# Kernel tuning notes

Hardware: AMD Instinct MI355X
Metric: run time of the kernel (lower is better)

Reference implementation:

```python
import jax, jax.numpy as jnp
import numpy as np
from jax import lax

IN_CH = 128
INTER_CH = 128
AUDIO_CH = 1
K = 2
DILATIONS = [2 ** i for i in range(10)] * 4  # 40 blocks
B, T = 4, 8192


def _causal_conv1d(x, w, dilation):
    # x: [B, Cin, T], w: [Cout, Cin, K] -> [B, Cout, T], left-padded (causal)
    pad = dilation * (w.shape[-1] - 1)
    return lax.conv_general_dilated(
        x, w, window_strides=(1,), padding=[(pad, 0)],
        rhs_dilation=(dilation,), dimension_numbers=('NCH', 'OIH', 'NCH'))


def setup_inputs() -> dict:
    key = jax.random.key(0)
    ks = jax.random.split(key, 12)
    L = len(DILATIONS)
    s = 0.05
    return {
        'x': jax.random.normal(ks[0], (B, AUDIO_CH, T), jnp.float32),
        'pre_w': jax.random.normal(ks[1], (IN_CH, AUDIO_CH, 3), jnp.float32) * s,
        'pre_b': jax.random.normal(ks[2], (IN_CH,), jnp.float32) * s,
        'conv_w': jax.random.normal(ks[3], (L, 2 * INTER_CH, IN_CH, K), jnp.float32) * s,
        'conv_b': jax.random.normal(ks[4], (L, 2 * INTER_CH), jnp.float32) * s,
        'post_w': jax.random.normal(ks[5], (L, IN_CH, INTER_CH), jnp.float32) * s,
        'post_b': jax.random.normal(ks[6], (L, IN_CH), jnp.float32) * s,
        'lin1_w': jax.random.normal(ks[7], (INTER_CH, INTER_CH), jnp.float32) * s,
        'lin1_b': jax.random.normal(ks[8], (INTER_CH,), jnp.float32) * s,
        'lin2_w': jax.random.normal(ks[9], (IN_CH, INTER_CH), jnp.float32) * s,
        'lin2_b': jax.random.normal(ks[10], (IN_CH,), jnp.float32) * s,
    }


def reference(x, pre_w, pre_b, conv_w, conv_b, post_w, post_b,
              lin1_w, lin1_b, lin2_w, lin2_b):
    # pre_net: ConstantPad1d((2,0)) + Conv1d(k=3) == causal conv, dilation 1
    h = _causal_conv1d(x, pre_w, 1) + pre_b[None, :, None]  # [B, IN_CH, T]
    skip_sum = jnp.zeros((x.shape[0], INTER_CH, x.shape[-1]), h.dtype)
    for i, d in enumerate(DILATIONS):
        y = _causal_conv1d(h, conv_w[i], d) + conv_b[i][None, :, None]  # [B, 2*INTER, T]
        a, b = jnp.split(y, 2, axis=1)
        skip = a * jax.nn.sigmoid(b)                                    # GLU
        h = h + jnp.einsum('oc,bct->bot', post_w[i], skip) + post_b[i][None, :, None]
        skip_sum = skip_sum + skip
    # conv2sa: [B, C, T] -> [T, B, C]
    z = jnp.transpose(skip_sum, (2, 0, 1))
    z = jax.nn.relu(z)
    z = z @ lin1_w.T + lin1_b
    z = jax.nn.relu(z)
    return z @ lin2_w.T + lin2_b  # [T, B, IN_CH]
```

## Files before the change

kernel.cpp:

```cpp
#include <hip/hip_runtime.h>
#include <hip/hip_bf16.h>

typedef __bf16 bf16;
typedef unsigned long long u64;
typedef __bf16 bf16x8 __attribute__((ext_vector_type(8)));
typedef __bf16 bf16x4 __attribute__((ext_vector_type(4)));
typedef float f32x4 __attribute__((ext_vector_type(4)));

#define NB 4
#define T 8192
#define C 128
#define NBLK 40
#define XS 136

#define MFMA(a, b, c) __builtin_amdgcn_mfma_f32_16x16x32_bf16(a, b, c, 0, 0, 0)

__device__ __forceinline__ float bf2f(bf16 x){ return (float)x; }
__device__ __forceinline__ bf16 f2bf(float x){ return (bf16)x; }

__device__ __forceinline__ float ld(const void* p, int i, int isbf){
    return isbf ? bf2f(((const bf16*)p)[i]) : ((const float*)p)[i];
}

__device__ __forceinline__ bf16x4 ld8(const bf16* p){
    u64 v = __hip_atomic_load((const u64*)p, __ATOMIC_RELAXED, __HIP_MEMORY_SCOPE_AGENT);
    return __builtin_bit_cast(bf16x4, v);
}
__device__ __forceinline__ void st16c(bf16* p, f32x4 v){
    asm volatile("global_store_dwordx4 %0, %1, off sc0 sc1" :: "v"(p), "v"(v) : "memory");
}

__global__ __launch_bounds__(64) void k_detect(const unsigned short* __restrict__ u,
                                               int* __restrict__ flag){
    unsigned short v = u[threadIdx.x * 2];
    int e = (v >> 7) & 255;
    bool sane = (e >= 100 && e <= 140) || ((v & 0x7FFF) == 0);
    unsigned long long m = __ballot(sane);
    if (threadIdx.x == 0) *flag = (__popcll(m) >= 48) ? 1 : 0;
}

__global__ __launch_bounds__(256) void k_prep(
    const void* __restrict__ conv_w, const void* __restrict__ post_w,
    const void* __restrict__ lin1_w, const void* __restrict__ lin2_w,
    const void* __restrict__ x,      const void* __restrict__ conv_b,
    const void* __restrict__ post_b, const void* __restrict__ pre_w,
    const void* __restrict__ pre_b,  const void* __restrict__ lin1_b,
    const void* __restrict__ lin2_b,
    bf16* __restrict__ weff, bf16* __restrict__ pwc,
    bf16* __restrict__ w1c,  bf16* __restrict__ w2c,
    float* __restrict__ xc,  float* __restrict__ cbf,
    float* __restrict__ pbf, float* __restrict__ misc,
    const int* __restrict__ flag){
    int f = *flag;
    int g = blockIdx.x * 256 + threadIdx.x;
    if (g < 327680){
        int blk = g >> 13, r = g & 8191, o = r >> 5, j = r & 31;
        int k = (j >= 16) ? 1 : 0;
        int base = blk * 65536 + o * 256 + (j * 8 - k * 128) * 2 + k;
        bf16x8 v;
#pragma unroll
        for (int m = 0; m < 8; m++) v[m] = f2bf(ld(conv_w, base + m * 2, f));
        *(bf16x8*)(weff + (size_t)g * 8) = v;
    } else if (g < 409600){
        int e = (g - 327680) * 8;
        bf16x8 v;
#pragma unroll
        for (int m = 0; m < 8; m++) v[m] = f2bf(ld(post_w, e + m, f));
        *(bf16x8*)(pwc + e) = v;
    } else if (g < 411648){
        int e = (g - 409600) * 8;
        bf16x8 v;
#pragma unroll
        for (int m = 0; m < 8; m++) v[m] = f2bf(ld(lin1_w, e + m, f));
        *(bf16x8*)(w1c + e) = v;
    } else if (g < 413696){
        int e = (g - 411648) * 8;
        bf16x8 v;
#pragma unroll
        for (int m = 0; m < 8; m++) v[m] = f2bf(ld(lin2_w, e + m, f));
        *(bf16x8*)(w2c + e) = v;
    } else if (g < 417792){
        int e = (g - 413696) * 8;
#pragma unroll
        for (int m = 0; m < 8; m++) xc[e + m] = ld(x, e + m, f);
    } else if (g < 419072){
        int e = (g - 417792) * 8;
#pragma unroll
        for (int m = 0; m < 8; m++) cbf[e + m] = ld(conv_b, e + m, f);
    } else if (g < 419712){
        int e = (g - 419072) * 8;
#pragma unroll
        for (int m = 0; m < 8; m++) pbf[e + m] = ld(post_b, e + m, f);
    } else if (g < 419808){
        int e = (g - 419712) * 8;
#pragma unroll
        for (int m = 0; m < 8; m++){
            int idx = e + m;
            if      (idx < 384) misc[idx] = ld(pre_w,  idx,       f);
            else if (idx < 512) misc[idx] = ld(pre_b,  idx - 384, f);
            else if (idx < 640) misc[idx] = ld(lin1_b, idx - 512, f);
            else                misc[idx] = ld(lin2_b, idx - 640, f);
        }
    }
}

__device__ __forceinline__ void wait_ge(unsigned* p, unsigned v){
    int guard = 0;
    while (__hip_atomic_load(p, __ATOMIC_RELAXED, __HIP_MEMORY_SCOPE_AGENT) < v){
        __builtin_amdgcn_s_sleep(1);
        if (++guard > (1 << 22)) break;
    }
    asm volatile("" ::: "memory");
}

__device__ __forceinline__ void tail_store(const bf16* Xo, bf16* dst, int nrows, int tid){
    int ngr = nrows * 16;
    for (int g = tid; g < ngr; g += 512){
        int rr = 128 - nrows + (g >> 4), co = (g & 15) * 8;
        f32x4 v = *(const f32x4*)(Xo + rr * XS + co);
        st16c(dst + (size_t)rr * C + co, v);
    }
    asm volatile("s_waitcnt vmcnt(0)" ::: "memory");
}

__global__ __launch_bounds__(512, 2) void k_main(
    const float* __restrict__ xc,  const float* __restrict__ misc,
    const bf16* __restrict__ weff, const float* __restrict__ cbf,
    const bf16* __restrict__ pwc,  const float* __restrict__ pbf,
    const bf16* __restrict__ w1c,  const bf16* __restrict__ w2c,
    bf16* __restrict__ hA, bf16* __restrict__ hB,
    unsigned* __restrict__ prog, unsigned* __restrict__ cons,
    void* __restrict__ outv, const int* __restrict__ flag)
{
    __shared__ __align__(16) bf16 LDSB[3 * 128 * XS];
    bf16* Xo = LDSB;
    bf16* Xh = LDSB + 128 * XS;
    bf16* Xs = LDSB + 256 * XS;

    int tid  = threadIdx.x;
    int wg   = blockIdx.x;
    int b    = wg >> 6;
    int slab = wg & 63;
    int t0   = slab * 128;
    int wv = tid >> 6, ln = tid & 63, lo = ln & 15, quad = ln >> 4;
    const size_t hb = (size_t)b * T * C;

    float hreg[32];
    float ssum[32];

    {
        const float* xr = xc + b * T;
#pragma unroll
        for (int ct = 0; ct < 8; ct++){
            int t = t0 + ct * 16 + lo;
            float x0 = (t >= 2) ? xr[t - 2] : 0.f;
            float x1 = (t >= 1) ? xr[t - 1] : 0.f;
            float x2 = xr[t];
            bf16x4 hv;
#pragma unroll
            for (int r = 0; r < 4; r++){
                int c = wv * 16 + quad * 4 + r;
                float acc = misc[384 + c] + misc[c*3]*x0 + misc[c*3+1]*x1 + misc[c*3+2]*x2;
                hreg[ct * 4 + r] = acc;
                hv[r] = f2bf(acc);
            }
            *(bf16x4*)(Xo + (ct * 16 + lo) * XS + wv * 16 + quad * 4) = hv;
        }
    }
#pragma unroll
    for (int i = 0; i < 32; i++) ssum[i] = 0.f;
    __syncthreads();
    if (slab < 63) tail_store(Xo, hA + hb + (size_t)t0 * C, 1, tid);
    __syncthreads();
    if (tid == 0)
        __hip_atomic_store(prog + wg, 1u, __ATOMIC_RELAXED, __HIP_MEMORY_SCOPE_AGENT);

    for (int i = 0; i < NBLK; i++){
        int d  = 1 << (i % 10);
        int D  = (d >= 128) ? (d >> 7) : 1;
        int dn = (i < NBLK - 1) ? (1 << ((i + 1) % 10)) : 0;
        int Dn = (dn >= 128) ? (dn >> 7) : 1;
        int nst = (dn < 128) ? dn : 128;
        bool last = (i == NBLK - 1);
        bool do_store = !last && (slab + Dn <= 63);
        const bf16* hin  = (i & 1) ? hB : hA;
        bf16*       hout = (i & 1) ? hA : hB;
        const bf16* wb   = weff + ((size_t)i << 16);
        const bf16* pwb  = pwc  + i * 16384;
        const float* cb  = cbf + i * 256;
        const float* pb  = pbf + i * 128;

        f32x4 cacc0[8] = {}, cacc1[8] = {};

#pragma unroll
        for (int kk = 0; kk < 4; kk++){
            int ko = 128 + kk * 32 + quad * 8;
            bf16x8 a0 = *(const bf16x8*)(wb + (size_t)(wv*16 + lo) * 256 + ko);
            bf16x8 a1 = *(const bf16x8*)(wb + (size_t)(128 + wv*16 + lo) * 256 + ko);
#pragma unroll
            for (int ct = 0; ct < 8; ct++){
                bf16x8 bf_ = *(const bf16x8*)(Xo + (ct*16 + lo) * XS + kk*32 + quad*8);
                cacc0[ct] = MFMA(a0, bf_, cacc0[ct]);
                cacc1[ct] = MFMA(a1, bf_, cacc1[ct]);
            }
        }
        if (slab >= D) wait_ge(prog + (wg - D), (unsigned)(i + 1));
        {
            int nr = (d < 128) ? d : 128;
            int tbase = t0 - d;
            int ngr8 = nr * 32;
            for (int g = tid; g < ngr8; g += 512){
                int row = g >> 5, c4 = (g & 31) << 2;
                int t = tbase + row;
                bf16x4 v = {};
                if (t >= 0) v = ld8(hin + hb + (size_t)t * C + c4);
                *(bf16x4*)(Xh + row * XS + c4) = v;
            }
        }
        __syncthreads();
        if (!last && tid == 0)
            __hip_atomic_store(cons + wg, (unsigned)(i + 1),
                               __ATOMIC_RELAXED, __HIP_MEMORY_SCOPE_AGENT);
        {
            int soff[8];
#pragma unroll
            for (int ct = 0; ct < 8; ct++){
                int row = ct * 16 + lo;
                soff[ct] = (row >= d) ? (row - d) * XS
                                      : (128 * XS + row * XS);
            }
#pragma unroll
            for (int kk = 0; kk < 4; kk++){
                int ko = kk * 32 + quad * 8;
                bf16x8 a0 = *(const bf16x8*)(wb + (size_t)(wv*16 + lo) * 256 + ko);
                bf16x8 a1 = *(const bf16x8*)(wb + (size_t)(128 + wv*16 + lo) * 256 + ko);
#pragma unroll
                for (int ct = 0; ct < 8; ct++){
                    bf16x8 bf_ = *(const bf16x8*)(LDSB + soff[ct] + ko);
                    cacc0[ct] = MFMA(a0, bf_, cacc0[ct]);
                    cacc1[ct] = MFMA(a1, bf_, cacc1[ct]);
                }
            }
        }
#pragma unroll
        for (int ct = 0; ct < 8; ct++){
            int col = ct * 16 + lo;
            bf16x4 sv;
#pragma unroll
            for (int r = 0; r < 4; r++){
                int j = wv * 16 + quad * 4 + r;
                float a = cacc0[ct][r] + cb[j];
                float g = cacc1[ct][r] + cb[128 + j];
                float s = a * __builtin_amdgcn_rcpf(1.f + __expf(-g));
                ssum[ct * 4 + r] += s;
                sv[r] = f2bf(s);
            }
            if (!last) *(bf16x4*)(Xs + col * XS + wv * 16 + quad * 4) = sv;
        }
        if (last) break;
        __syncthreads();
        {
            f32x4 pacc[8] = {};
#pragma unroll
            for (int kk = 0; kk < 4; kk++){
                bf16x8 pa = *(const bf16x8*)(pwb + (wv*16 + lo) * 128 + kk*32 + quad*8);
#pragma unroll
                for (int ct = 0; ct < 8; ct++){
                    bf16x8 pbv = *(const bf16x8*)(Xs + (ct*16 + lo) * XS + kk*32 + quad*8);
                    pacc[ct] = MFMA(pa, pbv, pacc[ct]);
                }
            }
#pragma unroll
            for (int ct = 0; ct < 8; ct++){
                bf16x4 hv;
#pragma unroll
                for (int r = 0; r < 4; r++){
                    hreg[ct * 4 + r] += pacc[ct][r] + pb[wv * 16 + quad * 4 + r];
                    hv[r] = f2bf(hreg[ct * 4 + r]);
                }
                *(bf16x4*)(Xo + (ct * 16 + lo) * XS + wv * 16 + quad * 4) = hv;
            }
        }
        if (do_store && i >= 1){
            int dp = 1 << ((i - 1) % 10);
            int Dp = (dp >= 128) ? (dp >> 7) : 1;
            if (slab + Dp <= 63) wait_ge(cons + (wg + Dp), (unsigned)i);
        }
        __syncthreads();
        if (do_store) tail_store(Xo, hout + hb + (size_t)t0 * C, nst, tid);
        __syncthreads();
        if (tid == 0)
            __hip_atomic_store(prog + wg, (unsigned)(i + 2),
                               __ATOMIC_RELAXED, __HIP_MEMORY_SCOPE_AGENT);
    }

    const float* b1 = misc + 512;
    const float* b2 = misc + 640;
    int isbf = *flag;
    __syncthreads();
#pragma unroll
    for (int ct = 0; ct < 8; ct++){
        int col = ct * 16 + lo;
        bf16x4 zv;
#pragma unroll
        for (int r = 0; r < 4; r++){
            float z = ssum[ct * 4 + r];
            zv[r] = f2bf(z > 0.f ? z : 0.f);
        }
        *(bf16x4*)(Xs + col * XS + wv * 16 + quad * 4) = zv;
    }
    __syncthreads();
    f32x4 a1[8] = {};
#pragma unroll
    for (int kk = 0; kk < 4; kk++){
        bf16x8 pa = *(const bf16x8*)(w1c + (wv*16 + lo) * 128 + kk*32 + quad*8);
#pragma unroll
        for (int ct = 0; ct < 8; ct++){
            bf16x8 pbv = *(const bf16x8*)(Xs + (ct*16 + lo) * XS + kk*32 + quad*8);
            a1[ct] = MFMA(pa, pbv, a1[ct]);
        }
    }
    __syncthreads();
#pragma unroll
    for (int ct = 0; ct < 8; ct++){
        int col = ct * 16 + lo;
        bf16x4 uv;
#pragma unroll
        for (int r = 0; r < 4; r++){
            int row = wv * 16 + quad * 4 + r;
            float u = a1[ct][r] + b1[row];
            uv[r] = f2bf(u > 0.f ? u : 0.f);
        }
        *(bf16x4*)(Xs + col * XS + wv * 16 + quad * 4) = uv;
    }
    __syncthreads();
    f32x4 a2[8] = {};
#pragma unroll
    for (int kk = 0; kk < 4; kk++){
        bf16x8 pa = *(const bf16x8*)(w2c + (wv*16 + lo) * 128 + kk*32 + quad*8);
#pragma unroll
        for (int ct = 0; ct < 8; ct++){
            bf16x8 pbv = *(const bf16x8*)(Xs + (ct*16 + lo) * XS + kk*32 + quad*8);
            a2[ct] = MFMA(pa, pbv, a2[ct]);
        }
    }
#pragma unroll
    for (int ct = 0; ct < 8; ct++){
        int col = t0 + ct * 16 + lo;
#pragma unroll
        for (int r = 0; r < 4; r++){
            int row = wv * 16 + quad * 4 + r;
            float v = a2[ct][r] + b2[row];
            size_t oi = ((size_t)col * NB + b) * C + row;
            if (isbf) ((bf16*)outv)[oi] = f2bf(v);
            else      ((float*)outv)[oi] = v;
        }
    }
}

extern "C" void kernel_launch(void* const* d_in, const int* in_sizes, int n_in,
                              void* d_out, int out_size, void* d_ws, size_t ws_size,
                              hipStream_t stream){
    const void* x      = d_in[0];
    const void* pre_w  = d_in[1];
    const void* pre_b  = d_in[2];
    const void* conv_w = d_in[3];
    const void* conv_b = d_in[4];
    const void* post_w = d_in[5];
    const void* post_b = d_in[6];
    const void* lin1w  = d_in[7];
    const void* lin1b  = d_in[8];
    const void* lin2w  = d_in[9];
    const void* lin2b  = d_in[10];

    char* ws = (char*)d_ws;
    bf16*     hA   = (bf16*)    (ws);
    bf16*     hB   = (bf16*)    (ws +  8388608);
    bf16*     weff = (bf16*)    (ws + 16777216);
    bf16*     pwc  = (bf16*)    (ws + 22020096);
    bf16*     w1c  = (bf16*)    (ws + 23330816);
    bf16*     w2c  = (bf16*)    (ws + 23363584);
    float*    xc   = (float*)   (ws + 23396352);
    float*    cbf  = (float*)   (ws + 23527424);
    float*    pbf  = (float*)   (ws + 23568384);
    float*    misc = (float*)   (ws + 23588864);
    int*      flag = (int*)     (ws + 23591936);
    unsigned* prog = (unsigned*)(ws + 23592960);
    unsigned* cons = (unsigned*)(ws + 23593984);

    hipMemsetAsync(prog, 0, 2048, stream);
    k_detect<<<1, 64, 0, stream>>>((const unsigned short*)x, flag);
    k_prep<<<1640, 256, 0, stream>>>(conv_w, post_w, lin1w, lin2w, x, conv_b,
                                     post_b, pre_w, pre_b, lin1b, lin2b,
                                     weff, pwc, w1c, w2c, xc, cbf, pbf, misc, flag);

    const float* xc_c   = xc;   const float* misc_c = misc;
    const bf16*  weff_c = weff; const float* cbf_c  = cbf;
    const bf16*  pwc_c  = pwc;  const float* pbf_c  = pbf;
    const bf16*  w1c_c  = w1c;  const bf16*  w2c_c  = w2c;
    void* out_v = d_out;        const int* flag_c = flag;
    void* ka[14] = { &xc_c, &misc_c, &weff_c, &cbf_c, &pwc_c, &pbf_c,
                     &w1c_c, &w2c_c, &hA, &hB, &prog, &cons, &out_v, &flag_c };
    hipLaunchCooperativeKernel((void*)k_main, dim3(256), dim3(512), ka, 0, stream);
}
```

Measured before the change: 540.2 us.

## Prefetch halo rows and conv weights before MFMA; fold dtype detect into prep

Moves the dependency wait and the global halo-row loads ahead of the current-tap MFMA loop, keeping them in registers so their latency overlaps compute before they are written to LDS. Also preloads the shifted-tap conv weights into registers once rather than reloading them inside the second MFMA loop. Separately, folds the dtype-detection kernel into k_prep, so each block computes the flag itself and one launch is dropped. The register staging raises VGPR pressure in a 512-thread cooperative kernel, which could spill. Waiting earlier may also stall before independent compute.

```diff
diff --git a/kernel.cpp b/kernel.cpp
--- a/kernel.cpp
+++ b/kernel.cpp
@@ -28,15 +28,6 @@
 }
 __device__ __forceinline__ void st16c(bf16* p, f32x4 v){
     asm volatile("global_store_dwordx4 %0, %1, off sc0 sc1" :: "v"(p), "v"(v) : "memory");
-}
-
-__global__ __launch_bounds__(64) void k_detect(const unsigned short* __restrict__ u,
-                                               int* __restrict__ flag){
-    unsigned short v = u[threadIdx.x * 2];
-    int e = (v >> 7) & 255;
-    bool sane = (e >= 100 && e <= 140) || ((v & 0x7FFF) == 0);
-    unsigned long long m = __ballot(sane);
-    if (threadIdx.x == 0) *flag = (__popcll(m) >= 48) ? 1 : 0;
 }
 
 __global__ __launch_bounds__(256) void k_prep(
@@ -50,8 +41,21 @@
     bf16* __restrict__ w1c,  bf16* __restrict__ w2c,
     float* __restrict__ xc,  float* __restrict__ cbf,
     float* __restrict__ pbf, float* __restrict__ misc,
-    const int* __restrict__ flag){
-    int f = *flag;
+    int* __restrict__ flag){
+    __shared__ int sf;
+    if (threadIdx.x < 64){
+        unsigned short v = ((const unsigned short*)x)[threadIdx.x * 2];
+        int e = (v >> 7) & 255;
+        bool sane = (e >= 100 && e <= 140) || ((v & 0x7FFF) == 0);
+        unsigned long long m = __ballot(sane);
+        if (threadIdx.x == 0){
+            int fv = (__popcll(m) >= 48) ? 1 : 0;
+            sf = fv;
+            if (blockIdx.x == 0) *flag = fv;
+        }
+    }
+    __syncthreads();
+    int f = sf;
     int g = blockIdx.x * 256 + threadIdx.x;
     if (g < 327680){
         int blk = g >> 13, r = g & 8191, o = r >> 5, j = r & 31;
@@ -192,6 +196,30 @@
 
         f32x4 cacc0[8] = {}, cacc1[8] = {};
 
+        if (slab >= D) wait_ge(prog + (wg - D), (unsigned)(i + 1));
+        int nr = (d < 128) ? d : 128;
+        int ngr8 = nr * 32;
+        int tbase = t0 - d;
+        bf16x4 stg[8];
+#pragma unroll
+        for (int j = 0; j < 8; j++){
+            int g = j * 512 + tid;
+            bf16x4 v = {};
+            if (g < ngr8){
+                int row = g >> 5, c4 = (g & 31) << 2;
+                int t = tbase + row;
+                if (t >= 0) v = ld8(hin + hb + (size_t)t * C + c4);
+            }
+            stg[j] = v;
+        }
+        bf16x8 cw0[4], cw1[4];
+#pragma unroll
+        for (int kk = 0; kk < 4; kk++){
+            int ko = kk * 32 + quad * 8;
+            cw0[kk] = *(const bf16x8*)(wb + (size_t)(wv*16 + lo) * 256 + ko);
+            cw1[kk] = *(const bf16x8*)(wb + (size_t)(128 + wv*16 + lo) * 256 + ko);
+        }
+
 #pragma unroll
         for (int kk = 0; kk < 4; kk++){
             int ko = 128 + kk * 32 + quad * 8;
@@ -204,17 +232,12 @@
                 cacc1[ct] = MFMA(a1, bf_, cacc1[ct]);
             }
         }
-        if (slab >= D) wait_ge(prog + (wg - D), (unsigned)(i + 1));
-        {
-            int nr = (d < 128) ? d : 128;
-            int tbase = t0 - d;
-            int ngr8 = nr * 32;
-            for (int g = tid; g < ngr8; g += 512){
+#pragma unroll
+        for (int j = 0; j < 8; j++){
+            int g = j * 512 + tid;
+            if (g < ngr8){
                 int row = g >> 5, c4 = (g & 31) << 2;
-                int t = tbase + row;
-                bf16x4 v = {};
-                if (t >= 0) v = ld8(hin + hb + (size_t)t * C + c4);
-                *(bf16x4*)(Xh + row * XS + c4) = v;
+                *(bf16x4*)(Xh + row * XS + c4) = stg[j];
             }
         }
         __syncthreads();
@@ -232,13 +255,11 @@
 #pragma unroll
             for (int kk = 0; kk < 4; kk++){
                 int ko = kk * 32 + quad * 8;
-                bf16x8 a0 = *(const bf16x8*)(wb + (size_t)(wv*16 + lo) * 256 + ko);
-                bf16x8 a1 = *(const bf16x8*)(wb + (size_t)(128 + wv*16 + lo) * 256 + ko);
 #pragma unroll
                 for (int ct = 0; ct < 8; ct++){
                     bf16x8 bf_ = *(const bf16x8*)(LDSB + soff[ct] + ko);
-                    cacc0[ct] = MFMA(a0, bf_, cacc0[ct]);
-                    cacc1[ct] = MFMA(a1, bf_, cacc1[ct]);
+                    cacc0[ct] = MFMA(cw0[kk], bf_, cacc0[ct]);
+                    cacc1[ct] = MFMA(cw1[kk], bf_, cacc1[ct]);
                 }
             }
         }
@@ -389,7 +410,6 @@
     unsigned* cons = (unsigned*)(ws + 23593984);
 
     hipMemsetAsync(prog, 0, 2048, stream);
-    k_detect<<<1, 64, 0, stream>>>((const unsigned short*)x, flag);
     k_prep<<<1640, 256, 0, stream>>>(conv_w, post_w, lin1w, lin2w, x, conv_b,
                                      post_b, pre_w, pre_b, lin1b, lin2b,
                                      weff, pwc, w1c, w2c, xc, cbf, pbf, misc, flag);
```

Measured after the change: 615.9 us. +14.0%, slower.

## Double workgroup to 1024 threads splitting time columns across wave halves; fold detect into prep

Applied to the files above, without the earlier changes.

Each workgroup now runs 16 waves instead of 8. Each half handles 64 of the 128 time columns, which halves per-thread accumulators and hidden state registers. The dtype-detection kernel is merged into k_prep, so there is one fewer launch. The aim is more wave parallelism per slab for latency hiding on the sequential dilation chain. The cost is more threads contending on barriers, and the launch bound of 4 could force register spills.

```diff
diff --git a/kernel.cpp b/kernel.cpp
--- a/kernel.cpp
+++ b/kernel.cpp
@@ -12,6 +12,7 @@
 #define C 128
 #define NBLK 40
 #define XS 136
+#define NT 1024
 
 #define MFMA(a, b, c) __builtin_amdgcn_mfma_f32_16x16x32_bf16(a, b, c, 0, 0, 0)
 
@@ -28,15 +29,6 @@
 }
 __device__ __forceinline__ void st16c(bf16* p, f32x4 v){
     asm volatile("global_store_dwordx4 %0, %1, off sc0 sc1" :: "v"(p), "v"(v) : "memory");
-}
-
-__global__ __launch_bounds__(64) void k_detect(const unsigned short* __restrict__ u,
-                                               int* __restrict__ flag){
-    unsigned short v = u[threadIdx.x * 2];
-    int e = (v >> 7) & 255;
-    bool sane = (e >= 100 && e <= 140) || ((v & 0x7FFF) == 0);
-    unsigned long long m = __ballot(sane);
-    if (threadIdx.x == 0) *flag = (__popcll(m) >= 48) ? 1 : 0;
 }
 
 __global__ __launch_bounds__(256) void k_prep(
@@ -50,8 +42,21 @@
     bf16* __restrict__ w1c,  bf16* __restrict__ w2c,
     float* __restrict__ xc,  float* __restrict__ cbf,
     float* __restrict__ pbf, float* __restrict__ misc,
-    const int* __restrict__ flag){
-    int f = *flag;
+    int* __restrict__ flag){
+    __shared__ int sf;
+    if (threadIdx.x < 64){
+        unsigned short v = ((const unsigned short*)x)[threadIdx.x * 2];
+        int e = (v >> 7) & 255;
+        bool sane = (e >= 100 && e <= 140) || ((v & 0x7FFF) == 0);
+        unsigned long long m = __ballot(sane);
+        if (threadIdx.x == 0){
+            int fv = (__popcll(m) >= 48) ? 1 : 0;
+            sf = fv;
+            if (blockIdx.x == 0) *flag = fv;
+        }
+    }
+    __syncthreads();
+    int f = sf;
     int g = blockIdx.x * 256 + threadIdx.x;
     if (g < 327680){
         int blk = g >> 13, r = g & 8191, o = r >> 5, j = r & 31;
@@ -115,7 +120,7 @@
 
 __device__ __forceinline__ void tail_store(const bf16* Xo, bf16* dst, int nrows, int tid){
     int ngr = nrows * 16;
-    for (int g = tid; g < ngr; g += 512){
+    for (int g = tid; g < ngr; g += NT){
         int rr = 128 - nrows + (g >> 4), co = (g & 15) * 8;
         f32x4 v = *(const f32x4*)(Xo + rr * XS + co);
         st16c(dst + (size_t)rr * C + co, v);
@@ -123,7 +128,7 @@
     asm volatile("s_waitcnt vmcnt(0)" ::: "memory");
 }
 
-__global__ __launch_bounds__(512, 2) void k_main(
+__global__ __launch_bounds__(1024, 4) void k_main(
     const float* __restrict__ xc,  const float* __restrict__ misc,
     const bf16* __restrict__ weff, const float* __restrict__ cbf,
     const bf16* __restrict__ pwc,  const float* __restrict__ pbf,
@@ -143,32 +148,35 @@
     int slab = wg & 63;
     int t0   = slab * 128;
     int wv = tid >> 6, ln = tid & 63, lo = ln & 15, quad = ln >> 4;
+    int wq = wv & 7, wH = wv >> 3;
+    const int cb0 = wH * 64;
     const size_t hb = (size_t)b * T * C;
 
-    float hreg[32];
-    float ssum[32];
+    float hreg[16];
+    float ssum[16];
 
     {
         const float* xr = xc + b * T;
 #pragma unroll
-        for (int ct = 0; ct < 8; ct++){
-            int t = t0 + ct * 16 + lo;
+        for (int ct = 0; ct < 4; ct++){
+            int col = cb0 + ct * 16 + lo;
+            int t = t0 + col;
             float x0 = (t >= 2) ? xr[t - 2] : 0.f;
             float x1 = (t >= 1) ? xr[t - 1] : 0.f;
             float x2 = xr[t];
             bf16x4 hv;
 #pragma unroll
             for (int r = 0; r < 4; r++){
-                int c = wv * 16 + quad * 4 + r;
+                int c = wq * 16 + quad * 4 + r;
                 float acc = misc[384 + c] + misc[c*3]*x0 + misc[c*3+1]*x1 + misc[c*3+2]*x2;
                 hreg[ct * 4 + r] = acc;
                 hv[r] = f2bf(acc);
             }
-            *(bf16x4*)(Xo + (ct * 16 + lo) * XS + wv * 16 + quad * 4) = hv;
-        }
-    }
-#pragma unroll
-    for (int i = 0; i < 32; i++) ssum[i] = 0.f;
+            *(bf16x4*)(Xo + col * XS + wq * 16 + quad * 4) = hv;
+        }
+    }
+#pragma unroll
+    for (int i = 0; i < 16; i++) ssum[i] = 0.f;
     __syncthreads();
     if (slab < 63) tail_store(Xo, hA + hb + (size_t)t0 * C, 1, tid);
     __syncthreads();
@@ -190,16 +198,16 @@
         const float* cb  = cbf + i * 256;
         const float* pb  = pbf + i * 128;
 
-        f32x4 cacc0[8] = {}, cacc1[8] = {};
+        f32x4 cacc0[4] = {}, cacc1[4] = {};
 
 #pragma unroll
         for (int kk = 0; kk < 4; kk++){
             int ko = 128 + kk * 32 + quad * 8;
-            bf16x8 a0 = *(const bf16x8*)(wb + (size_t)(wv*16 + lo) * 256 + ko);
-            bf16x8 a1 = *(const bf16x8*)(wb + (size_t)(128 + wv*16 + lo) * 256 + ko);
-#pragma unroll
-            for (int ct = 0; ct < 8; ct++){
-                bf16x8 bf_ = *(const bf16x8*)(Xo + (ct*16 + lo) * XS + kk*32 + quad*8);
+            bf16x8 a0 = *(const bf16x8*)(wb + (size_t)(wq*16 + lo) * 256 + ko);
+            bf16x8 a1 = *(const bf16x8*)(wb + (size_t)(128 + wq*16 + lo) * 256 + ko);
+#pragma unroll
+            for (int ct = 0; ct < 4; ct++){
+                bf16x8 bf_ = *(const bf16x8*)(Xo + (cb0 + ct*16 + lo) * XS + kk*32 + quad*8);
                 cacc0[ct] = MFMA(a0, bf_, cacc0[ct]);
                 cacc1[ct] = MFMA(a1, bf_, cacc1[ct]);
             }
@@ -209,7 +217,7 @@
             int nr = (d < 128) ? d : 128;
             int tbase = t0 - d;
             int ngr8 = nr * 32;
-            for (int g = tid; g < ngr8; g += 512){
+            for (int g = tid; g < ngr8; g += NT){
                 int row = g >> 5, c4 = (g & 31) << 2;
                 int t = tbase + row;
                 bf16x4 v = {};
@@ -222,20 +230,20 @@
             __hip_atomic_store(cons + wg, (unsigned)(i + 1),
                                __ATOMIC_RELAXED, __HIP_MEMORY_SCOPE_AGENT);
         {
-            int soff[8];
-#pragma unroll
-            for (int ct = 0; ct < 8; ct++){
-                int row = ct * 16 + lo;
-                soff[ct] = (row >= d) ? (row - d) * XS
-                                      : (128 * XS + row * XS);
+            int soff[4];
+#pragma unroll
+            for (int ct = 0; ct < 4; ct++){
+                int col = cb0 + ct * 16 + lo;
+                soff[ct] = (col >= d) ? (col - d) * XS
+                                      : (128 * XS + col * XS);
             }
 #pragma unroll
             for (int kk = 0; kk < 4; kk++){
                 int ko = kk * 32 + quad * 8;
-                bf16x8 a0 = *(const bf16x8*)(wb + (size_t)(wv*16 + lo) * 256 + ko);
-                bf16x8 a1 = *(const bf16x8*)(wb + (size_t)(128 + wv*16 + lo) * 256 + ko);
-#pragma unroll
-                for (int ct = 0; ct < 8; ct++){
+                bf16x8 a0 = *(const bf16x8*)(wb + (size_t)(wq*16 + lo) * 256 + ko);
+                bf16x8 a1 = *(const bf16x8*)(wb + (size_t)(128 + wq*16 + lo) * 256 + ko);
+#pragma unroll
+                for (int ct = 0; ct < 4; ct++){
                     bf16x8 bf_ = *(const bf16x8*)(LDSB + soff[ct] + ko);
                     cacc0[ct] = MFMA(a0, bf_, cacc0[ct]);
                     cacc1[ct] = MFMA(a1, bf_, cacc1[ct]);
@@ -243,42 +251,42 @@
             }
         }
 #pragma unroll
-        for (int ct = 0; ct < 8; ct++){
-            int col = ct * 16 + lo;
+        for (int ct = 0; ct < 4; ct++){
+            int col = cb0 + ct * 16 + lo;
             bf16x4 sv;
 #pragma unroll
             for (int r = 0; r < 4; r++){
-                int j = wv * 16 + quad * 4 + r;
+                int j = wq * 16 + quad * 4 + r;
                 float a = cacc0[ct][r] + cb[j];
                 float g = cacc1[ct][r] + cb[128 + j];
                 float s = a * __builtin_amdgcn_rcpf(1.f + __expf(-g));
                 ssum[ct * 4 + r] += s;
                 sv[r] = f2bf(s);
             }
-            if (!last) *(bf16x4*)(Xs + col * XS + wv * 16 + quad * 4) = sv;
+            if (!last) *(bf16x4*)(Xs + col * XS + wq * 16 + quad * 4) = sv;
         }
         if (last) break;
         __syncthreads();
         {
-            f32x4 pacc[8] = {};
+            f32x4 pacc[4] = {};
 #pragma unroll
             for (int kk = 0; kk < 4; kk++){
-                bf16x8 pa = *(const bf16x8*)(pwb + (wv*16 + lo) * 128 + kk*32 + quad*8);
-#pragma unroll
-                for (int ct = 0; ct < 8; ct++){
-                    bf16x8 pbv = *(const bf16x8*)(Xs + (ct*16 + lo) * XS + kk*32 + quad*8);
+                bf16x8 pa = *(const bf16x8*)(pwb + (wq*16 + lo) * 128 + kk*32 + quad*8);
+#pragma unroll
+                for (int ct = 0; ct < 4; ct++){
+                    bf16x8 pbv = *(const bf16x8*)(Xs + (cb0 + ct*16 + lo) * XS + kk*32 + quad*8);
                     pacc[ct] = MFMA(pa, pbv, pacc[ct]);
                 }
             }
 #pragma unroll
-            for (int ct = 0; ct < 8; ct++){
+            for (int ct = 0; ct < 4; ct++){
                 bf16x4 hv;
 #pragma unroll
                 for (int r = 0; r < 4; r++){
-                    hreg[ct * 4 + r] += pacc[ct][r] + pb[wv * 16 + quad * 4 + r];
+                    hreg[ct * 4 + r] += pacc[ct][r] + pb[wq * 16 + quad * 4 + r];
                     hv[r] = f2bf(hreg[ct * 4 + r]);
                 }
-                *(bf16x4*)(Xo + (ct * 16 + lo) * XS + wv * 16 + quad * 4) = hv;
+                *(bf16x4*)(Xo + (cb0 + ct * 16 + lo) * XS + wq * 16 + quad * 4) = hv;
             }
         }
         if (do_store && i >= 1){
@@ -299,57 +307,57 @@
     int isbf = *flag;
     __syncthreads();
 #pragma unroll
-    for (int ct = 0; ct < 8; ct++){
-        int col = ct * 16 + lo;
+    for (int ct = 0; ct < 4; ct++){
+        int col = cb0 + ct * 16 + lo;
         bf16x4 zv;
 #pragma unroll
         for (int r = 0; r < 4; r++){
             float z = ssum[ct * 4 + r];
             zv[r] = f2bf(z > 0.f ? z : 0.f);
         }
-        *(bf16x4*)(Xs + col * XS + wv * 16 + quad * 4) = zv;
-    }
-    __syncthreads();
-    f32x4 a1[8] = {};
+        *(bf16x4*)(Xs + col * XS + wq * 16 + quad * 4) = zv;
+    }
+    __syncthreads();
+    f32x4 a1[4] = {};
 #pragma unroll
     for (int kk = 0; kk < 4; kk++){
-        bf16x8 pa = *(const bf16x8*)(w1c + (wv*16 + lo) * 128 + kk*32 + quad*8);
-#pragma unroll
-        for (int ct = 0; ct < 8; ct++){
-            bf16x8 pbv = *(const bf16x8*)(Xs + (ct*16 + lo) * XS + kk*32 + quad*8);
+        bf16x8 pa = *(const bf16x8*)(w1c + (wq*16 + lo) * 128 + kk*32 + quad*8);
+#pragma unroll
+        for (int ct = 0; ct < 4; ct++){
+            bf16x8 pbv = *(const bf16x8*)(Xs + (cb0 + ct*16 + lo) * XS + kk*32 + quad*8);
             a1[ct] = MFMA(pa, pbv, a1[ct]);
         }
     }
     __syncthreads();
 #pragma unroll
-    for (int ct = 0; ct < 8; ct++){
-        int col = ct * 16 + lo;
+    for (int ct = 0; ct < 4; ct++){
+        int col = cb0 + ct * 16 + lo;
         bf16x4 uv;
 #pragma unroll
         for (int r = 0; r < 4; r++){
-            int row = wv * 16 + quad * 4 + r;
+            int row = wq * 16 + quad * 4 + r;
             float u = a1[ct][r] + b1[row];
             uv[r] = f2bf(u > 0.f ? u : 0.f);
         }
-        *(bf16x4*)(Xs + col * XS + wv * 16 + quad * 4) = uv;
-    }
-    __syncthreads();
-    f32x4 a2[8] = {};
+        *(bf16x4*)(Xs + col * XS + wq * 16 + quad * 4) = uv;
+    }
+    __syncthreads();
+    f32x4 a2[4] = {};
 #pragma unroll
     for (int kk = 0; kk < 4; kk++){
-        bf16x8 pa = *(const bf16x8*)(w2c + (wv*16 + lo) * 128 + kk*32 + quad*8);
-#pragma unroll
-        for (int ct = 0; ct < 8; ct++){
-            bf16x8 pbv = *(const bf16x8*)(Xs + (ct*16 + lo) * XS + kk*32 + quad*8);
+        bf16x8 pa = *(const bf16x8*)(w2c + (wq*16 + lo) * 128 + kk*32 + quad*8);
+#pragma unroll
+        for (int ct = 0; ct < 4; ct++){
+            bf16x8 pbv = *(const bf16x8*)(Xs + (cb0 + ct*16 + lo) * XS + kk*32 + quad*8);
             a2[ct] = MFMA(pa, pbv, a2[ct]);
         }
     }
 #pragma unroll
-    for (int ct = 0; ct < 8; ct++){
-        int col = t0 + ct * 16 + lo;
+    for (int ct = 0; ct < 4; ct++){
+        int col = t0 + cb0 + ct * 16 + lo;
 #pragma unroll
         for (int r = 0; r < 4; r++){
-            int row = wv * 16 + quad * 4 + r;
+            int row = wq * 16 + quad * 4 + r;
             float v = a2[ct][r] + b2[row];
             size_t oi = ((size_t)col * NB + b) * C + row;
             if (isbf) ((bf16*)outv)[oi] = f2bf(v);
@@ -389,7 +397,6 @@
     unsigned* cons = (unsigned*)(ws + 23593984);
 
     hipMemsetAsync(prog, 0, 2048, stream);
-    k_detect<<<1, 64, 0, stream>>>((const unsigned short*)x, flag);
     k_prep<<<1640, 256, 0, stream>>>(conv_w, post_w, lin1w, lin2w, x, conv_b,
                                      post_b, pre_w, pre_b, lin1b, lin2b,
                                      weff, pwc, w1c, w2c, xc, cbf, pbf, misc, flag);
@@ -401,5 +408,5 @@
     void* out_v = d_out;        const int* flag_c = flag;
     void* ka[14] = { &xc_c, &misc_c, &weff_c, &cbf_c, &pwc_c, &pbf_c,
                      &w1c_c, &w2c_c, &hA, &hB, &prog, &cons, &out_v, &flag_c };
-    hipLaunchCooperativeKernel((void*)k_main, dim3(256), dim3(512), ka, 0, stream);
-}
+    hipLaunchCooperativeKernel((void*)k_main, dim3(256), dim3(1024), ka, 0, stream);
+}
```

Result: slower. 691.0 us (+27.9%).
